# Performance work log

Measured on AMD Instinct MI355X. Metric: run time of the kernel, lower is better.

## Reference

```python
import jax, jax.numpy as jnp
import numpy as np

N = 50000      # nodes
E = 300000     # edges per relation
IN = 128       # in_feats
HF = 64        # h_feats
AH = 4         # att_heads
R = 3          # relations
H = HF * AH    # 256, per-relation hidden width


def setup_inputs() -> dict:
    key = jax.random.key(0)
    ks = jax.random.split(key, 10)
    s = 0.05
    h = jax.random.normal(ks[0], (N, IN), jnp.float32)
    # relation_aware params (shared across relations)
    dW = jax.random.normal(ks[1], (IN, H), jnp.float32) * s
    db = jnp.zeros((H,), jnp.float32)
    fW = jax.random.normal(ks[2], (3 * H, 1), jnp.float32) * s
    fb = jnp.zeros((1,), jnp.float32)
    # per-relation H2FDLayer params (stacked over R)
    wW = jax.random.normal(ks[3], (R, IN, H), jnp.float32) * s
    wb = jnp.zeros((R, H), jnp.float32)
    aW = jax.random.normal(ks[4], (R, 2 * HF, 1), jnp.float32) * s
    ab = jnp.zeros((R, 1), jnp.float32)
    # final combining linear
    linW = jax.random.normal(ks[5], (R * H, H), jnp.float32) * s
    linb = jnp.zeros((H,), jnp.float32)
    src = jax.random.randint(ks[6], (R, E), 0, N, jnp.int32)
    dst = jax.random.randint(ks[7], (R, E), 0, N, jnp.int32)
    return dict(h=h, dW=dW, db=db, fW=fW, fb=fb, wW=wW, wb=wb,
                aW=aW, ab=ab, linW=linW, linb=linb, src=src, dst=dst)


def _segment_softmax(alpha, seg, num_segments):
    # alpha: [E, AH]; softmax over edges sharing the same destination node
    amax = jax.ops.segment_max(alpha, seg, num_segments=num_segments)
    ex = jnp.exp(alpha - amax[seg])
    denom = jax.ops.segment_sum(ex, seg, num_segments=num_segments)
    return ex / denom[seg]


def reference(h, dW, db, fW, fb, wW, wb, aW, ab, linW, linb, src, dst):
    hd = h @ dW + db  # [N, H] relation_aware d_liner (shared)
    outs = []
    for r in range(R):
        s_idx, d_idx = src[r], dst[r]
        sd, dd = hd[s_idx], hd[d_idx]  # [E, H]
        # sign_edges: tanh(f_liner(cat[src,dst,src-dst])) -> sign
        score = jnp.tanh((jnp.concatenate([sd, dd, sd - dd], axis=1) @ fW + fb)[:, 0])
        sign = jnp.sign(score)  # [E]
        hw = h @ wW[r] + wb[r]  # [N, H] per-relation w_liner
        sf = (sign[:, None] * hw[s_idx]).reshape(E, AH, HF)          # signed src features
        z = jnp.concatenate([sf, hw[d_idx].reshape(E, AH, HF)], -1)  # [E, AH, 2*HF]
        alpha = jax.nn.leaky_relu((z @ aW[r] + ab[r])[..., 0], 0.01)  # [E, AH]
        w = _segment_softmax(alpha, d_idx, N)                         # [E, AH]
        out_r = jax.ops.segment_sum(w[..., None] * sf, d_idx, num_segments=N)
        outs.append(out_r.reshape(N, H))
    out = jnp.concatenate(outs, axis=1)  # [N, R*H]
    return out @ linW + linb             # [N, H]
```

## Files before the change

### kernel.cpp

```cpp
#include <hip/hip_runtime.h>

#define NN 50000
#define MP 50048
#define EE 300000
#define KIN 128
#define HH 256
#define KOUT 768
#define NAH 4
#define NHF 64
#define NR 3

#define GSH 7
#define NG 391
#define NBKT (NR * NG)
#define BCAP 1024
#define EPB 16384
#define NTOT (NR * EE)

typedef __attribute__((ext_vector_type(8))) short short8_t;
typedef __attribute__((ext_vector_type(4))) float f32x4;

#define O_DBL   0ull
#define O_GS    2080ull
#define O_GD    202080ull
#define O_ASRC  402080ull
#define O_ADST  2802080ull
#define O_GCNT  5202080ull
#define O_GBUF  5210272ull
#define O_H16   10014880ull
#define O_WT    22827168ull
#define O_LWT   23023776ull
#define O_HW16  23416992ull
#define O_OUTA  100290720ull

__device__ __forceinline__ ushort f2bf(float x) {
  union { float f; unsigned u; } c; c.f = x;
  return (ushort)((c.u + 0x7FFFu + ((c.u >> 16) & 1u)) >> 16);
}
__device__ __forceinline__ float bf2f(ushort u) {
  return __uint_as_float(((unsigned)u) << 16);
}

__global__ void k_prep(const float* __restrict__ dW, const float* __restrict__ db,
                       const float* __restrict__ fW, double* __restrict__ dbuf) {
  int t = threadIdx.x;
  if (t < KIN) {
    double p = 0.0, q = 0.0;
    for (int j = 0; j < HH; ++j) {
      double u = (double)fW[j] + (double)fW[2 * HH + j];
      double v = (double)fW[HH + j] - (double)fW[2 * HH + j];
      double w = (double)dW[t * HH + j];
      p += w * u; q += w * v;
    }
    dbuf[t] = p; dbuf[KIN + t] = q;
  } else if (t == KIN) {
    double cu = 0.0, cv = 0.0;
    for (int j = 0; j < HH; ++j) {
      double u = (double)fW[j] + (double)fW[2 * HH + j];
      double v = (double)fW[HH + j] - (double)fW[2 * HH + j];
      cu += (double)db[j] * u; cv += (double)db[j] * v;
    }
    dbuf[2 * KIN] = cu; dbuf[2 * KIN + 1] = cv;
  }
}

__global__ __launch_bounds__(256) void k_fuse(const float* __restrict__ h,
                                              const double* __restrict__ dbuf,
                                              float* __restrict__ gs, float* __restrict__ gd,
                                              ushort* __restrict__ h16) {
  int bid = blockIdx.x;
  if (bid == NN / 4) {
    for (int i = threadIdx.x; i < (MP - NN) * KIN / 8; i += 256) {
      short8_t z = {0, 0, 0, 0, 0, 0, 0, 0};
      *(short8_t*)&h16[(size_t)NN * KIN + i * 8] = z;
    }
    return;
  }
  int node = (int)((bid * 256u + threadIdx.x) >> 6);
  int lane = threadIdx.x & 63;
  float2 hv = *(const float2*)&h[(size_t)node * KIN + lane * 2];
  ushort2 o2; o2.x = f2bf(hv.x); o2.y = f2bf(hv.y);
  *(ushort2*)&h16[(size_t)node * KIN + lane * 2] = o2;
  double ps = (double)hv.x * dbuf[lane * 2] + (double)hv.y * dbuf[lane * 2 + 1];
  double qs = (double)hv.x * dbuf[KIN + lane * 2] + (double)hv.y * dbuf[KIN + lane * 2 + 1];
#pragma unroll
  for (int m = 32; m; m >>= 1) { ps += __shfl_xor(ps, m, 64); qs += __shfl_xor(qs, m, 64); }
  if (lane == 0) {
    gs[node] = (float)(ps + dbuf[2 * KIN]);
    gd[node] = (float)(qs + dbuf[2 * KIN + 1]);
  }
}

#define WT_ELEMS (NR * HH * KIN)
#define LWT_ELEMS (HH * KOUT)
__global__ __launch_bounds__(256) void k_cvtW(const float* __restrict__ wW, const float* __restrict__ linW,
                                              ushort* __restrict__ Wt, ushort* __restrict__ LWt) {
  int t = blockIdx.x * 256 + threadIdx.x;
  if (t < WT_ELEMS) {
    int r = t / (HH * KIN), rem = t % (HH * KIN);
    int n = rem / KIN, k = rem % KIN;
    Wt[t] = f2bf(wW[((size_t)r * KIN + k) * HH + n]);
  }
  int u = t - WT_ELEMS;
  if (u >= 0 && u < LWT_ELEMS) {
    int n = u / KOUT, kk = u % KOUT;
    LWt[u] = f2bf(linW[(size_t)kk * HH + n]);
  }
}

template <int K, bool BIAS, bool OBF16>
__global__ __launch_bounds__(256) void k_mm(const ushort* __restrict__ A0,
                                            const ushort* __restrict__ Bt0,
                                            const float* __restrict__ bias0,
                                            void* __restrict__ Cv, int M, int bStride,
                                            size_t btZ, size_t biasZ, size_t cZ) {
  __shared__ ushort As[128][40];
  __shared__ ushort Bs[128][40];
  const ushort* A = A0;
  const ushort* Bt = Bt0 + (size_t)blockIdx.z * btZ;
  const float* bias = BIAS ? bias0 + (size_t)blockIdx.z * biasZ : bias0;
  size_t cOfs = (size_t)blockIdx.z * cZ;
  int bm = blockIdx.x * 128, bn = blockIdx.y * 128;
  int tid = threadIdx.x, lane = tid & 63, w = tid >> 6;
  int wm = w >> 1, wn = w & 1;
  int sr = tid >> 2, sk = (tid & 3) * 8;
  int fr = lane & 15, kb = (lane >> 4) * 8;
  const bool aok0 = (bm + sr) < M, aok1 = (bm + 64 + sr) < M;
  f32x4 acc[4][4] = {};
  for (int k0 = 0; k0 < K; k0 += 32) {
    short8_t a0 = {0, 0, 0, 0, 0, 0, 0, 0}, a1 = {0, 0, 0, 0, 0, 0, 0, 0};
    if (aok0) a0 = *(const short8_t*)&A[(size_t)(bm + sr) * K + k0 + sk];
    if (aok1) a1 = *(const short8_t*)&A[(size_t)(bm + 64 + sr) * K + k0 + sk];
    short8_t b0 = *(const short8_t*)&Bt[(size_t)(bn + sr) * bStride + k0 + sk];
    short8_t b1 = *(const short8_t*)&Bt[(size_t)(bn + 64 + sr) * bStride + k0 + sk];
    __syncthreads();
    *(short8_t*)&As[sr][sk] = a0;
    *(short8_t*)&As[64 + sr][sk] = a1;
    *(short8_t*)&Bs[sr][sk] = b0;
    *(short8_t*)&Bs[64 + sr][sk] = b1;
    __syncthreads();
    short8_t af[4], bfr[4];
#pragma unroll
    for (int i = 0; i < 4; ++i) af[i] = *(const short8_t*)&As[wm * 64 + i * 16 + fr][kb];
#pragma unroll
    for (int i = 0; i < 4; ++i) bfr[i] = *(const short8_t*)&Bs[wn * 64 + i * 16 + fr][kb];
#pragma unroll
    for (int i = 0; i < 4; ++i)
#pragma unroll
      for (int j = 0; j < 4; ++j)
        acc[i][j] = __builtin_amdgcn_mfma_f32_16x16x32_bf16(af[i], bfr[j], acc[i][j], 0, 0, 0);
  }
  int rq = lane >> 4;
#pragma unroll
  for (int i = 0; i < 4; ++i) {
#pragma unroll
    for (int j = 0; j < 4; ++j) {
      int col = bn + wn * 64 + j * 16 + fr;
      float bv = 0.f;
      if constexpr (BIAS) bv = bias[col];
#pragma unroll
      for (int q = 0; q < 4; ++q) {
        int row = bm + wm * 64 + i * 16 + rq * 4 + q;
        if (row < M) {
          float v = acc[i][j][q] + bv;
          if constexpr (OBF16) ((ushort*)Cv)[cOfs + (size_t)row * HH + col] = f2bf(v);
          else ((float*)Cv)[(size_t)row * HH + col] = v;
        }
      }
    }
  }
}

__global__ __launch_bounds__(256) void k_aproj(const ushort* __restrict__ hwAll,
                                               const float* __restrict__ aWAll,
                                               float* __restrict__ asrcAll,
                                               float* __restrict__ adstAll) {
  int r = blockIdx.y;
  const ushort* hw = hwAll + (size_t)r * MP * HH;
  const float* aW = aWAll + (size_t)r * 2 * NHF;
  int node = (int)((blockIdx.x * 256u + threadIdx.x) >> 6);
  int lane = threadIdx.x & 63;
  if (node >= NN) return;
  int ah = lane >> 4, j = lane & 15;
  ushort4 hv4 = *(const ushort4*)&hw[(size_t)node * HH + ah * NHF + j * 4];
  float hx = bf2f(hv4.x), hy = bf2f(hv4.y), hz = bf2f(hv4.z), hwv = bf2f(hv4.w);
  float4 a1 = *(const float4*)&aW[j * 4];
  float4 a2 = *(const float4*)&aW[NHF + j * 4];
  float s1 = hx * a1.x + hy * a1.y + hz * a1.z + hwv * a1.w;
  float s2 = hx * a2.x + hy * a2.y + hz * a2.z + hwv * a2.w;
#pragma unroll
  for (int m = 8; m; m >>= 1) { s1 += __shfl_xor(s1, m, 64); s2 += __shfl_xor(s2, m, 64); }
  if (j == 0) {
    asrcAll[(size_t)r * NN * NAH + (size_t)node * NAH + ah] = s1;
    adstAll[(size_t)r * NN * NAH + (size_t)node * NAH + ah] = s2;
  }
}

__global__ __launch_bounds__(512) void k_bin(const int* __restrict__ dst,
                                             const int* __restrict__ src,
                                             int* __restrict__ gcnt,
                                             uint* __restrict__ gbuf) {
  __shared__ int hist[NBKT];
  __shared__ int base[NBKT];
  int tid = threadIdx.x;
  int start = blockIdx.x * EPB;
  for (int b = tid; b < NBKT; b += 512) hist[b] = 0;
  __syncthreads();
#pragma unroll 4
  for (int i = 0; i < EPB / 512; ++i) {
    int e = start + i * 512 + tid;
    if (e < NTOT) {
      int d = dst[e];
      int r = (e >= 2 * EE) ? 2 : ((e >= EE) ? 1 : 0);
      atomicAdd(&hist[r * NG + (d >> GSH)], 1);
    }
  }
  __syncthreads();
  for (int b = tid; b < NBKT; b += 512) {
    int c = hist[b];
    base[b] = (c > 0) ? atomicAdd(&gcnt[b], c) : 0;
    hist[b] = 0;
  }
  __syncthreads();
#pragma unroll 4
  for (int i = 0; i < EPB / 512; ++i) {
    int e = start + i * 512 + tid;
    if (e < NTOT) {
      int d = dst[e];
      int sv = src[e];
      int r = (e >= 2 * EE) ? 2 : ((e >= EE) ? 1 : 0);
      int bkt = r * NG + (d >> GSH);
      int idx = base[bkt] + atomicAdd(&hist[bkt], 1);
      if (idx < BCAP)
        gbuf[(size_t)bkt * BCAP + idx] = ((uint)(d & 127) << 17) | (uint)sv;
    }
  }
}

__global__ __launch_bounds__(512) void k_edgeB(const ushort* __restrict__ hwAll,
                                               const float* __restrict__ gs,
                                               const float* __restrict__ gd,
                                               const float* __restrict__ asrcAll,
                                               const float* __restrict__ adstAll,
                                               const float* __restrict__ fb,
                                               const float* __restrict__ abAll,
                                               const int* __restrict__ gcnt,
                                               const uint* __restrict__ gbuf,
                                               ushort* __restrict__ out768) {
  __shared__ uint ebuf[BCAP];
  __shared__ uint csr[BCAP];
  __shared__ float gsv[BCAP];
  __shared__ ushort asv[BCAP * 4];
  __shared__ int cntL[128], offL[128], curL[128];
  int rl = blockIdx.x / NG, g = blockIdx.x % NG;
  const ushort* hw = hwAll + (size_t)rl * MP * HH;
  const float* asrc = asrcAll + (size_t)rl * NN * NAH;
  const float* adst = adstAll + (size_t)rl * NN * NAH;
  int tid = threadIdx.x;
  int cb = gcnt[blockIdx.x]; if (cb > BCAP) cb = BCAP;
  if (tid < 128) { cntL[tid] = 0; curL[tid] = 0; }
  __syncthreads();
  for (int i = tid; i < cb; i += 512) {
    uint ent = gbuf[(size_t)blockIdx.x * BCAP + i];
    ebuf[i] = ent;
    atomicAdd(&cntL[ent >> 17], 1);
  }
  __syncthreads();
  if (tid < 64) {
    int c0 = cntL[2 * tid], c1 = cntL[2 * tid + 1];
    int s = c0 + c1, inc = s;
#pragma unroll
    for (int o = 1; o < 64; o <<= 1) {
      int v = __shfl_up(inc, o, 64);
      if (tid >= o) inc += v;
    }
    int ex = inc - s;
    offL[2 * tid] = ex;
    offL[2 * tid + 1] = ex + c0;
  }
  __syncthreads();
  for (int i = tid; i < cb; i += 512) {
    uint ent = ebuf[i];
    int b = (int)(ent >> 17);
    int idx = atomicAdd(&curL[b], 1);
    csr[offL[b] + idx] = ent;
  }
  __syncthreads();
  for (int i = tid; i < cb; i += 512) {
    int sv = (int)(csr[i] & 0x1FFFFu);
    gsv[i] = gs[sv];
    float4 a4 = *(const float4*)&asrc[(size_t)sv * NAH];
    ushort4 a16; a16.x = f2bf(a4.x); a16.y = f2bf(a4.y);
    a16.z = f2bf(a4.z); a16.w = f2bf(a4.w);
    *(ushort4*)&asv[4 * i] = a16;
  }
  __syncthreads();

  int lane = tid & 63, wv = tid >> 6;
  int head = lane >> 4, iE = lane >> 2, cah = lane & 3;
  float fbv = fb[0], abv = abAll[rl];
  size_t colBase = (size_t)rl * HH + lane * 4;
  for (int it = 0; it < 16; ++it) {
    int ln = wv + 8 * it;
    int node = (g << GSH) + ln;
    if (node >= NN) continue;
    int deg = cntL[ln]; deg = deg < 64 ? deg : 64;
    if (deg == 0) {
      ushort4 z = {0, 0, 0, 0};
      *(ushort4*)&out768[(size_t)node * KOUT + colBase] = z;
      continue;
    }
    int bofs = offL[ln];
    float gdn = gd[node];
    float adn = adst[(size_t)node * NAH + cah];
    float den = 0.f;
    float w_[4]; int s_[4];
#pragma unroll
    for (int p = 0; p < 4; ++p) {
      float wgt = 0.f; int sv = 0;
      if (p * 16 < deg) {
        int e = p * 16 + iE;
        float ex = 0.f;
        if (e < deg) {
          int i = bofs + e;
          sv = (int)(csr[i] & 0x1FFFFu);
          float t = gsv[i] + gdn + fbv;
          float sg = (t > 0.f) ? 1.f : ((t < 0.f) ? -1.f : 0.f);
          float a = sg * bf2f(asv[4 * i + cah]) + adn + abv;
          a = (a >= 0.f) ? a : 0.01f * a;
          ex = __expf(a);
          wgt = sg * ex;
        }
        float red = ex;
#pragma unroll
        for (int m = 4; m <= 32; m <<= 1) red += __shfl_xor(red, m, 64);
        den += red;
      }
      w_[p] = wgt; s_[p] = sv;
    }
    float rd = 1.f / __shfl(den, head, 64);
    float4 acc = {0, 0, 0, 0};
#pragma unroll
    for (int p = 0; p < 4; ++p) {
      if (p * 16 >= deg) break;
      int lim = deg - p * 16; lim = lim < 16 ? lim : 16;
      int i2 = 0;
      for (; i2 + 3 < lim; i2 += 4) {
        float w0 = __shfl(w_[p], i2 * 4 + head, 64);
        int   v0 = __shfl(s_[p], i2 * 4 + head, 64);
        float w1 = __shfl(w_[p], i2 * 4 + 4 + head, 64);
        int   v1 = __shfl(s_[p], i2 * 4 + 4 + head, 64);
        float w2 = __shfl(w_[p], i2 * 4 + 8 + head, 64);
        int   v2 = __shfl(s_[p], i2 * 4 + 8 + head, 64);
        float w3 = __shfl(w_[p], i2 * 4 + 12 + head, 64);
        int   v3 = __shfl(s_[p], i2 * 4 + 12 + head, 64);
        ushort4 h0 = *(const ushort4*)&hw[(size_t)v0 * HH + lane * 4];
        ushort4 h1 = *(const ushort4*)&hw[(size_t)v1 * HH + lane * 4];
        ushort4 h2 = *(const ushort4*)&hw[(size_t)v2 * HH + lane * 4];
        ushort4 h3 = *(const ushort4*)&hw[(size_t)v3 * HH + lane * 4];
        acc.x += w0 * bf2f(h0.x) + w1 * bf2f(h1.x) + w2 * bf2f(h2.x) + w3 * bf2f(h3.x);
        acc.y += w0 * bf2f(h0.y) + w1 * bf2f(h1.y) + w2 * bf2f(h2.y) + w3 * bf2f(h3.y);
        acc.z += w0 * bf2f(h0.z) + w1 * bf2f(h1.z) + w2 * bf2f(h2.z) + w3 * bf2f(h3.z);
        acc.w += w0 * bf2f(h0.w) + w1 * bf2f(h1.w) + w2 * bf2f(h2.w) + w3 * bf2f(h3.w);
      }
      for (; i2 < lim; ++i2) {
        float w0 = __shfl(w_[p], i2 * 4 + head, 64);
        int   v0 = __shfl(s_[p], i2 * 4 + head, 64);
        ushort4 h0 = *(const ushort4*)&hw[(size_t)v0 * HH + lane * 4];
        acc.x += w0 * bf2f(h0.x); acc.y += w0 * bf2f(h0.y);
        acc.z += w0 * bf2f(h0.z); acc.w += w0 * bf2f(h0.w);
      }
    }
    ushort4 o;
    o.x = f2bf(acc.x * rd); o.y = f2bf(acc.y * rd);
    o.z = f2bf(acc.z * rd); o.w = f2bf(acc.w * rd);
    *(ushort4*)&out768[(size_t)node * KOUT + colBase] = o;
  }
}

extern "C" void kernel_launch(void* const* d_in, const int* in_sizes, int n_in,
                              void* d_out, int out_size, void* d_ws, size_t ws_size,
                              hipStream_t stream) {
  const float* h    = (const float*)d_in[0];
  const float* dW   = (const float*)d_in[1];
  const float* db   = (const float*)d_in[2];
  const float* fW   = (const float*)d_in[3];
  const float* fb   = (const float*)d_in[4];
  const float* wW   = (const float*)d_in[5];
  const float* wb   = (const float*)d_in[6];
  const float* aW   = (const float*)d_in[7];
  const float* ab   = (const float*)d_in[8];
  const float* linW = (const float*)d_in[9];
  const float* linb = (const float*)d_in[10];
  const int*   src  = (const int*)d_in[11];
  const int*   dst  = (const int*)d_in[12];
  float* out = (float*)d_out;
  char* ws = (char*)d_ws;

  double* dbuf  = (double*)(ws + O_DBL);
  float* gs     = (float*)(ws + O_GS);
  float* gd     = (float*)(ws + O_GD);
  float* asrc   = (float*)(ws + O_ASRC);
  float* adst   = (float*)(ws + O_ADST);
  int*   gcnt   = (int*)(ws + O_GCNT);
  uint*  gbuf   = (uint*)(ws + O_GBUF);
  ushort* h16   = (ushort*)(ws + O_H16);
  ushort* Wt    = (ushort*)(ws + O_WT);
  ushort* LWt   = (ushort*)(ws + O_LWT);
  ushort* hw16  = (ushort*)(ws + O_HW16);
  ushort* out768 = (ushort*)(ws + O_OUTA);

  hipMemsetAsync(ws + O_GCNT, 0, 8192, stream);
  k_prep<<<1, 256, 0, stream>>>(dW, db, fW, dbuf);
  k_fuse<<<NN / 4 + 1, 256, 0, stream>>>(h, dbuf, gs, gd, h16);
  k_cvtW<<<(WT_ELEMS + LWT_ELEMS + 255) / 256, 256, 0, stream>>>(wW, linW, Wt, LWt);
  k_bin<<<(NTOT + EPB - 1) / EPB, 512, 0, stream>>>(dst, src, gcnt, gbuf);

  k_mm<KIN, true, true><<<dim3(MP / 128, 2, 3), 256, 0, stream>>>(
      h16, Wt, wb, hw16, MP, KIN, (size_t)HH * KIN, (size_t)HH, (size_t)MP * HH);
  k_aproj<<<dim3(NN / 4, 3), 256, 0, stream>>>(hw16, aW, asrc, adst);
  k_edgeB<<<NBKT, 512, 0, stream>>>(
      hw16, gs, gd, asrc, adst, fb, ab, gcnt, gbuf, out768);
  k_mm<KOUT, true, false><<<dim3(MP / 128, 2, 1), 256, 0, stream>>>(
      out768, LWt, linb, out, NN, KOUT, 0, 0, 0);
}
```

Measured before the change: 416.6 us.

## Use direct global-to-LDS loads in GEMM and merge setup kernels

The bf16 MFMA GEMM now loads its A and B tiles with global_load_lds, going straight from global memory into an unpadded LDS layout instead of through registers. The M-bound checks on A loads are removed, and the grid is reordered so the N tiles vary fastest. The weight conversion and the fW/dW precompute are folded into one kernel, and the gcnt memset moves into k_fuse, which cuts launch count. The unpadded LDS row stride may cause bank conflicts on fragment reads, and the unguarded A loads depend on the padded buffers being large enough.

Result: faster. 407.3 us (-2.2%).

```diff
diff --git a/kernel.cpp b/kernel.cpp
--- a/kernel.cpp
+++ b/kernel.cpp
@@ -40,40 +40,68 @@
 __device__ __forceinline__ float bf2f(ushort u) {
   return __uint_as_float(((unsigned)u) << 16);
 }
-
-__global__ void k_prep(const float* __restrict__ dW, const float* __restrict__ db,
-                       const float* __restrict__ fW, double* __restrict__ dbuf) {
-  int t = threadIdx.x;
-  if (t < KIN) {
-    double p = 0.0, q = 0.0;
-    for (int j = 0; j < HH; ++j) {
-      double u = (double)fW[j] + (double)fW[2 * HH + j];
-      double v = (double)fW[HH + j] - (double)fW[2 * HH + j];
-      double w = (double)dW[t * HH + j];
-      p += w * u; q += w * v;
-    }
-    dbuf[t] = p; dbuf[KIN + t] = q;
-  } else if (t == KIN) {
-    double cu = 0.0, cv = 0.0;
-    for (int j = 0; j < HH; ++j) {
-      double u = (double)fW[j] + (double)fW[2 * HH + j];
-      double v = (double)fW[HH + j] - (double)fW[2 * HH + j];
-      cu += (double)db[j] * u; cv += (double)db[j] * v;
-    }
-    dbuf[2 * KIN] = cu; dbuf[2 * KIN + 1] = cv;
+__device__ __forceinline__ void gl_lds16(const ushort* g, ushort* l) {
+  __builtin_amdgcn_global_load_lds(
+      (const __attribute__((address_space(1))) unsigned int*)g,
+      (__attribute__((address_space(3))) unsigned int*)l, 16, 0, 0);
+}
+
+#define WT_ELEMS (NR * HH * KIN)
+#define LWT_ELEMS (HH * KOUT)
+__global__ __launch_bounds__(256) void k_cvtP(const float* __restrict__ wW,
+                                              const float* __restrict__ linW,
+                                              const float* __restrict__ dW,
+                                              const float* __restrict__ db,
+                                              const float* __restrict__ fW,
+                                              ushort* __restrict__ Wt,
+                                              ushort* __restrict__ LWt,
+                                              double* __restrict__ dbuf) {
+  if (blockIdx.x == (WT_ELEMS + LWT_ELEMS) / 256) {
+    int t = threadIdx.x;
+    if (t < KIN) {
+      double p = 0.0, q = 0.0;
+      for (int j = 0; j < HH; ++j) {
+        double u = (double)fW[j] + (double)fW[2 * HH + j];
+        double v = (double)fW[HH + j] - (double)fW[2 * HH + j];
+        double w = (double)dW[t * HH + j];
+        p += w * u; q += w * v;
+      }
+      dbuf[t] = p; dbuf[KIN + t] = q;
+    } else if (t == KIN) {
+      double cu = 0.0, cv = 0.0;
+      for (int j = 0; j < HH; ++j) {
+        double u = (double)fW[j] + (double)fW[2 * HH + j];
+        double v = (double)fW[HH + j] - (double)fW[2 * HH + j];
+        cu += (double)db[j] * u; cv += (double)db[j] * v;
+      }
+      dbuf[2 * KIN] = cu; dbuf[2 * KIN + 1] = cv;
+    }
+    return;
+  }
+  int t = blockIdx.x * 256 + threadIdx.x;
+  if (t < WT_ELEMS) {
+    int r = t / (HH * KIN), rem = t % (HH * KIN);
+    int n = rem / KIN, k = rem % KIN;
+    Wt[t] = f2bf(wW[((size_t)r * KIN + k) * HH + n]);
+  } else {
+    int u = t - WT_ELEMS;
+    int n = u / KOUT, kk = u % KOUT;
+    LWt[u] = f2bf(linW[(size_t)kk * HH + n]);
   }
 }
 
 __global__ __launch_bounds__(256) void k_fuse(const float* __restrict__ h,
                                               const double* __restrict__ dbuf,
                                               float* __restrict__ gs, float* __restrict__ gd,
-                                              ushort* __restrict__ h16) {
+                                              ushort* __restrict__ h16,
+                                              int* __restrict__ gcnt) {
   int bid = blockIdx.x;
   if (bid == NN / 4) {
     for (int i = threadIdx.x; i < (MP - NN) * KIN / 8; i += 256) {
       short8_t z = {0, 0, 0, 0, 0, 0, 0, 0};
       *(short8_t*)&h16[(size_t)NN * KIN + i * 8] = z;
     }
+    for (int i = threadIdx.x; i < NBKT; i += 256) gcnt[i] = 0;
     return;
   }
   int node = (int)((bid * 256u + threadIdx.x) >> 6);
@@ -91,59 +119,43 @@
   }
 }
 
-#define WT_ELEMS (NR * HH * KIN)
-#define LWT_ELEMS (HH * KOUT)
-__global__ __launch_bounds__(256) void k_cvtW(const float* __restrict__ wW, const float* __restrict__ linW,
-                                              ushort* __restrict__ Wt, ushort* __restrict__ LWt) {
-  int t = blockIdx.x * 256 + threadIdx.x;
-  if (t < WT_ELEMS) {
-    int r = t / (HH * KIN), rem = t % (HH * KIN);
-    int n = rem / KIN, k = rem % KIN;
-    Wt[t] = f2bf(wW[((size_t)r * KIN + k) * HH + n]);
-  }
-  int u = t - WT_ELEMS;
-  if (u >= 0 && u < LWT_ELEMS) {
-    int n = u / KOUT, kk = u % KOUT;
-    LWt[u] = f2bf(linW[(size_t)kk * HH + n]);
-  }
-}
-
 template <int K, bool BIAS, bool OBF16>
-__global__ __launch_bounds__(256) void k_mm(const ushort* __restrict__ A0,
+__global__ __launch_bounds__(256) void k_mm(const ushort* __restrict__ A,
                                             const ushort* __restrict__ Bt0,
                                             const float* __restrict__ bias0,
-                                            void* __restrict__ Cv, int M, int bStride,
+                                            void* __restrict__ Cv, int M,
                                             size_t btZ, size_t biasZ, size_t cZ) {
-  __shared__ ushort As[128][40];
-  __shared__ ushort Bs[128][40];
-  const ushort* A = A0;
+  __shared__ ushort As[4096];
+  __shared__ ushort Bs[4096];
   const ushort* Bt = Bt0 + (size_t)blockIdx.z * btZ;
-  const float* bias = BIAS ? bias0 + (size_t)blockIdx.z * biasZ : bias0;
   size_t cOfs = (size_t)blockIdx.z * cZ;
-  int bm = blockIdx.x * 128, bn = blockIdx.y * 128;
+  int bn = blockIdx.x * 128, bm = blockIdx.y * 128;
   int tid = threadIdx.x, lane = tid & 63, w = tid >> 6;
   int wm = w >> 1, wn = w & 1;
-  int sr = tid >> 2, sk = (tid & 3) * 8;
   int fr = lane & 15, kb = (lane >> 4) * 8;
-  const bool aok0 = (bm + sr) < M, aok1 = (bm + 64 + sr) < M;
+  int srow = w * 16 + (lane >> 2);
+  int scol = (lane & 3) * 8;
+  ushort* lA0 = &As[w * 512];
+  ushort* lA1 = &As[2048 + w * 512];
+  ushort* lB0 = &Bs[w * 512];
+  ushort* lB1 = &Bs[2048 + w * 512];
+  const ushort* gA0 = &A[(size_t)(bm + srow) * K + scol];
+  const ushort* gA1 = &A[(size_t)(bm + 64 + srow) * K + scol];
+  const ushort* gB0 = &Bt[(size_t)(bn + srow) * K + scol];
+  const ushort* gB1 = &Bt[(size_t)(bn + 64 + srow) * K + scol];
   f32x4 acc[4][4] = {};
   for (int k0 = 0; k0 < K; k0 += 32) {
-    short8_t a0 = {0, 0, 0, 0, 0, 0, 0, 0}, a1 = {0, 0, 0, 0, 0, 0, 0, 0};
-    if (aok0) a0 = *(const short8_t*)&A[(size_t)(bm + sr) * K + k0 + sk];
-    if (aok1) a1 = *(const short8_t*)&A[(size_t)(bm + 64 + sr) * K + k0 + sk];
-    short8_t b0 = *(const short8_t*)&Bt[(size_t)(bn + sr) * bStride + k0 + sk];
-    short8_t b1 = *(const short8_t*)&Bt[(size_t)(bn + 64 + sr) * bStride + k0 + sk];
     __syncthreads();
-    *(short8_t*)&As[sr][sk] = a0;
-    *(short8_t*)&As[64 + sr][sk] = a1;
-    *(short8_t*)&Bs[sr][sk] = b0;
-    *(short8_t*)&Bs[64 + sr][sk] = b1;
+    gl_lds16(gA0 + k0, lA0);
+    gl_lds16(gA1 + k0, lA1);
+    gl_lds16(gB0 + k0, lB0);
+    gl_lds16(gB1 + k0, lB1);
     __syncthreads();
     short8_t af[4], bfr[4];
 #pragma unroll
-    for (int i = 0; i < 4; ++i) af[i] = *(const short8_t*)&As[wm * 64 + i * 16 + fr][kb];
-#pragma unroll
-    for (int i = 0; i < 4; ++i) bfr[i] = *(const short8_t*)&Bs[wn * 64 + i * 16 + fr][kb];
+    for (int i = 0; i < 4; ++i) af[i] = *(const short8_t*)&As[(wm * 64 + i * 16 + fr) * 32 + kb];
+#pragma unroll
+    for (int i = 0; i < 4; ++i) bfr[i] = *(const short8_t*)&Bs[(wn * 64 + i * 16 + fr) * 32 + kb];
 #pragma unroll
     for (int i = 0; i < 4; ++i)
 #pragma unroll
@@ -157,7 +169,7 @@
     for (int j = 0; j < 4; ++j) {
       int col = bn + wn * 64 + j * 16 + fr;
       float bv = 0.f;
-      if constexpr (BIAS) bv = bias[col];
+      if constexpr (BIAS) bv = bias0[(size_t)blockIdx.z * biasZ + col];
 #pragma unroll
       for (int q = 0; q < 4; ++q) {
         int row = bm + wm * 64 + i * 16 + rq * 4 + q;
@@ -410,17 +422,16 @@
   ushort* hw16  = (ushort*)(ws + O_HW16);
   ushort* out768 = (ushort*)(ws + O_OUTA);
 
-  hipMemsetAsync(ws + O_GCNT, 0, 8192, stream);
-  k_prep<<<1, 256, 0, stream>>>(dW, db, fW, dbuf);
-  k_fuse<<<NN / 4 + 1, 256, 0, stream>>>(h, dbuf, gs, gd, h16);
-  k_cvtW<<<(WT_ELEMS + LWT_ELEMS + 255) / 256, 256, 0, stream>>>(wW, linW, Wt, LWt);
+  k_cvtP<<<(WT_ELEMS + LWT_ELEMS) / 256 + 1, 256, 0, stream>>>(
+      wW, linW, dW, db, fW, Wt, LWt, dbuf);
+  k_fuse<<<NN / 4 + 1, 256, 0, stream>>>(h, dbuf, gs, gd, h16, gcnt);
   k_bin<<<(NTOT + EPB - 1) / EPB, 512, 0, stream>>>(dst, src, gcnt, gbuf);
 
-  k_mm<KIN, true, true><<<dim3(MP / 128, 2, 3), 256, 0, stream>>>(
-      h16, Wt, wb, hw16, MP, KIN, (size_t)HH * KIN, (size_t)HH, (size_t)MP * HH);
+  k_mm<KIN, true, true><<<dim3(2, MP / 128, 3), 256, 0, stream>>>(
+      h16, Wt, wb, hw16, MP, (size_t)HH * KIN, (size_t)HH, (size_t)MP * HH);
   k_aproj<<<dim3(NN / 4, 3), 256, 0, stream>>>(hw16, aW, asrc, adst);
   k_edgeB<<<NBKT, 512, 0, stream>>>(
       hw16, gs, gd, asrc, adst, fb, ab, gcnt, gbuf, out768);
-  k_mm<KOUT, true, false><<<dim3(MP / 128, 2, 1), 256, 0, stream>>>(
-      out768, LWt, linb, out, NN, KOUT, 0, 0, 0);
-}
+  k_mm<KOUT, true, false><<<dim3(2, MP / 128, 1), 256, 0, stream>>>(
+      out768, LWt, linb, out, NN, 0, 0, 0);
+}
```
